# Kernel optimization log

Measured on AMD Instinct MI355X. Metric: run time of the kernel, lower is better.

## Reference

```python
import jax, jax.numpy as jnp
import numpy as np
import math

RANKS = [16, 8, 4, 2, 1]          # generate_mrlora_ranks(32 // 2)
LORA_ALPHA = 16.0
SCALES = [LORA_ALPHA / math.sqrt(r) for r in RANKS]  # use_rslora=True
D_IN = 4096
D_OUT = 4096


def setup_inputs() -> dict:
    key = jax.random.key(0)
    ks = jax.random.split(key, 3 + 2 * len(RANKS))
    x = jax.random.normal(ks[0], (4, 2048, D_IN), dtype=jnp.float32)
    W = jax.random.normal(ks[1], (D_OUT, D_IN), dtype=jnp.float32) * (1.0 / math.sqrt(D_IN))
    b = jax.random.normal(ks[2], (D_OUT,), dtype=jnp.float32) * 0.01
    inp = {"x": x, "W": W, "b": b}
    for i, r in enumerate(RANKS):
        # A: [r, D_IN], B: [D_OUT, r] (torch nn.Linear weight layout)
        inp[f"A{r}"] = jax.random.normal(ks[3 + 2 * i], (r, D_IN), dtype=jnp.float32) * (1.0 / math.sqrt(D_IN))
        inp[f"B{r}"] = jax.random.normal(ks[4 + 2 * i], (D_OUT, r), dtype=jnp.float32) * 0.02
    inp["alphas"] = jnp.ones((len(RANKS),), dtype=jnp.float32)
    return inp


def reference(x, W, b, A16, B16, A8, B8, A4, B4, A2, B2, A1, B1, alphas):
    # base linear: x @ W.T + b
    out = jnp.einsum('bsd,od->bso', x, W) + b
    As = [A16, A8, A4, A2, A1]
    Bs = [B16, B8, B4, B2, B1]
    # dropout p=0 -> identity; per-rank low-rank update with learned + rslora scale
    for i, (A, B) in enumerate(zip(As, Bs)):
        coef = alphas[i] * SCALES[i]
        out = out + coef * jnp.einsum('bsr,or->bso', jnp.einsum('bsd,rd->bsr', x, A), B)
    return out
```

## Files before the change

### kernel.cpp

```cpp
#include <hip/hip_runtime.h>
#include <hip/hip_bf16.h>
#include <stdint.h>

#define DK 4096
#define MROWS 8192
#define NOUT 4096
#define KP 4160
#define KP_B (KP*2)
#define NT 65

typedef __attribute__((ext_vector_type(8))) __bf16 bf16x8;
typedef __attribute__((ext_vector_type(4))) float f32x4;
typedef unsigned short u16;

struct __align__(8) us4 { u16 x, y, z, w; };

__device__ __forceinline__ u16 f2bf(float f) {
  union { float f; uint32_t u; } v; v.f = f;
  uint32_t r = v.u + 0x7fffu + ((v.u >> 16) & 1u);
  return (u16)(r >> 16);
}

__device__ __forceinline__ void gload16(const void* g, void* l) {
  __builtin_amdgcn_global_load_lds(
      (const __attribute__((address_space(1))) unsigned int*)g,
      (__attribute__((address_space(3))) unsigned int*)l, 16, 0, 0);
}

__global__ void conv_x(const float* __restrict__ x, u16* __restrict__ xb) {
  int m = blockIdx.x, t = threadIdx.x;
  const float* src = x + (size_t)m * DK;
  u16* dst = xb + (size_t)m * KP;
#pragma unroll
  for (int j = 0; j < 4; ++j) {
    int col = (t + j * 256) * 4;
    float4 v = *reinterpret_cast<const float4*>(src + col);
    us4 o = { f2bf(v.x), f2bf(v.y), f2bf(v.z), f2bf(v.w) };
    *reinterpret_cast<us4*>(dst + col) = o;
  }
  if (t < 64) dst[4096 + t] = 0;
}

__global__ void build_W(const float* __restrict__ W,
                        const float* __restrict__ B16, const float* __restrict__ B8,
                        const float* __restrict__ B4,  const float* __restrict__ B2,
                        const float* __restrict__ B1,  const float* __restrict__ alphas,
                        u16* __restrict__ wb) {
  int n = blockIdx.x, t = threadIdx.x;
  const float* src = W + (size_t)n * DK;
  u16* dst = wb + (size_t)n * KP;
#pragma unroll
  for (int j = 0; j < 4; ++j) {
    int col = (t + j * 256) * 4;
    float4 v = *reinterpret_cast<const float4*>(src + col);
    us4 o = { f2bf(v.x), f2bf(v.y), f2bf(v.z), f2bf(v.w) };
    *reinterpret_cast<us4*>(dst + col) = o;
  }
  if (t < 64) {
    u16 val = 0;
    if (t < 31) {
      float coef; const float* Bp; int r, rl;
      if (t < 16)      { coef = alphas[0] * 4.0f;                Bp = B16; r = 16; rl = t; }
      else if (t < 24) { coef = alphas[1] * 5.656854249492381f;  Bp = B8;  r = 8;  rl = t - 16; }
      else if (t < 28) { coef = alphas[2] * 8.0f;                Bp = B4;  r = 4;  rl = t - 24; }
      else if (t < 30) { coef = alphas[3] * 11.313708498984761f; Bp = B2;  r = 2;  rl = t - 28; }
      else             { coef = alphas[4] * 16.0f;               Bp = B1;  r = 1;  rl = 0; }
      val = f2bf(coef * Bp[(size_t)n * r + rl]);
    }
    dst[4096 + t] = val;
  }
}

__global__ void build_A(const float* __restrict__ A16, const float* __restrict__ A8,
                        const float* __restrict__ A4,  const float* __restrict__ A2,
                        const float* __restrict__ A1,  u16* __restrict__ ab) {
  int rr = blockIdx.x, t = threadIdx.x;
  const float* src = nullptr;
  if (rr < 16)      src = A16 + (size_t)rr * DK;
  else if (rr < 24) src = A8 + (size_t)(rr - 16) * DK;
  else if (rr < 28) src = A4 + (size_t)(rr - 24) * DK;
  else if (rr < 30) src = A2 + (size_t)(rr - 28) * DK;
  else if (rr < 31) src = A1;
  u16* dst = ab + (size_t)rr * DK;
#pragma unroll
  for (int j = 0; j < 4; ++j) {
    int col = (t + j * 256) * 4;
    us4 o = { 0, 0, 0, 0 };
    if (src) {
      float4 v = *reinterpret_cast<const float4*>(src + col);
      o = { f2bf(v.x), f2bf(v.y), f2bf(v.z), f2bf(v.w) };
    }
    *reinterpret_cast<us4*>(dst + col) = o;
  }
}

__global__ __launch_bounds__(256, 2) void xa_gemm(u16* xb, const u16* __restrict__ ab) {
  __shared__ u16 Xs[64 * 64];
  __shared__ u16 Qs[32 * 64];
  int m0 = blockIdx.x * 64;
  int t = threadIdx.x, lane = t & 63, w = t >> 6;
  int l15 = lane & 15, lg = lane >> 4;
  f32x4 acc[2] = {};
  const char* xbase = (const char*)xb + (size_t)m0 * KP_B;
  for (int kt = 0; kt < 64; ++kt) {
    size_t kb = (size_t)kt * 128;
    __syncthreads();
#pragma unroll
    for (int i = 0; i < 2; ++i) {
      int chunk = w * 2 + i;
      int off = chunk * 1024 + lane * 16;
      int row = off >> 7, colB = off & 127;
      gload16(xbase + (size_t)row * KP_B + kb + colB, (char*)Xs + chunk * 1024);
    }
    {
      int off = w * 1024 + lane * 16;
      int row = off >> 7, colB = off & 127;
      gload16((const char*)ab + (size_t)row * (DK * 2) + kb + colB, (char*)Qs + w * 1024);
    }
    asm volatile("s_waitcnt vmcnt(0)" ::: "memory");
    __syncthreads();
#pragma unroll
    for (int ks = 0; ks < 2; ++ks) {
      bf16x8 xf = *reinterpret_cast<const bf16x8*>((const char*)Xs + (w * 16 + l15) * 128 + ks * 64 + lg * 16);
#pragma unroll
      for (int ni = 0; ni < 2; ++ni) {
        bf16x8 af = *reinterpret_cast<const bf16x8*>((const char*)Qs + (ni * 16 + l15) * 128 + ks * 64 + lg * 16);
        acc[ni] = __builtin_amdgcn_mfma_f32_16x16x32_bf16(xf, af, acc[ni], 0, 0, 0);
      }
    }
  }
#pragma unroll
  for (int ni = 0; ni < 2; ++ni)
#pragma unroll
    for (int r = 0; r < 4; ++r) {
      int m = m0 + w * 16 + lg * 4 + r;
      int c = 4096 + ni * 16 + l15;
      xb[(size_t)m * KP + c] = f2bf(acc[ni][r]);
    }
}

__device__ __forceinline__ void stage_tile(const char* gbase, char* lbase, int w, int lane, int i) {
  int chunk = (w << 2) + i;
  int row = (chunk << 3) + (lane >> 3);
  int src_c = ((lane & 7) ^ (lane >> 3)) << 4;
  gload16(gbase + (size_t)row * KP_B + src_c, lbase + chunk * 1024);
}

__device__ __forceinline__ bf16x8 rdfrag(const char* base, int row, int cb) {
  return *reinterpret_cast<const bf16x8*>(base + row * 128 + (cb ^ ((row & 7) << 4)));
}

__global__ __launch_bounds__(512, 2) void gemm_main(const u16* __restrict__ xb, const u16* __restrict__ wb,
                                                    const float* __restrict__ bias, float* __restrict__ out) {
  __shared__ u16 As0[256 * 64], As1[256 * 64];
  __shared__ u16 Bs0[256 * 64], Bs1[256 * 64];
  int bid = blockIdx.x;
  int swz = (bid & 7) * 64 + (bid >> 3);
  int mt = swz >> 4, nt = swz & 15;
  int m0 = mt * 256, n0 = nt * 256;
  int t = threadIdx.x, lane = t & 63, w = t >> 6;
  int wr = w >> 2, wc = w & 3;
  int l15 = lane & 15, lg = lane >> 4;

  f32x4 acc[8][4] = {};
  bf16x8 af[4][2], bl[2][2], bh[2][2];

  const char* Ag = (const char*)xb + (size_t)m0 * KP_B;
  const char* Bg = (const char*)wb + (size_t)n0 * KP_B;
  char *AcA = (char*)As0, *AnA = (char*)As1, *AcB = (char*)Bs0, *AnB = (char*)Bs1;

#pragma unroll
  for (int i = 0; i < 4; ++i) stage_tile(Bg, AcB, w, lane, i);
#pragma unroll
  for (int i = 0; i < 4; ++i) stage_tile(Ag, AcA, w, lane, i);
#pragma unroll
  for (int i = 0; i < 4; ++i) stage_tile(Bg + 128, AnB, w, lane, i);
  asm volatile("s_waitcnt vmcnt(4)" ::: "memory");
  __builtin_amdgcn_s_barrier();

  const int Arow = wr * 128 + l15;
  const int Brow = wc * 64 + l15;
  const int cb0 = lg * 16;

  for (int kt = 0; kt < NT; ++kt) {
    const char* Agk1 = Ag + (size_t)(kt + 1) * 128;
    const char* Bgk2 = Bg + (size_t)(kt + 2) * 128;
    const bool doA = (kt + 1 < NT), doB = (kt + 2 < NT);

#pragma unroll
    for (int mi = 0; mi < 4; ++mi)
#pragma unroll
      for (int ks = 0; ks < 2; ++ks)
        af[mi][ks] = rdfrag(AcA, Arow + mi * 16, cb0 + ks * 64);
#pragma unroll
    for (int ni = 0; ni < 2; ++ni)
#pragma unroll
      for (int ks = 0; ks < 2; ++ks)
        bl[ni][ks] = rdfrag(AcB, Brow + ni * 16, cb0 + ks * 64);
#pragma unroll
    for (int ni = 0; ni < 2; ++ni)
#pragma unroll
      for (int ks = 0; ks < 2; ++ks)
        bh[ni][ks] = rdfrag(AcB, Brow + 32 + ni * 16, cb0 + ks * 64);
    if (doA) {
      stage_tile(Agk1, AnA, w, lane, 0); stage_tile(Agk1, AnA, w, lane, 1);
      stage_tile(Agk1, AnA, w, lane, 2); stage_tile(Agk1, AnA, w, lane, 3);
    }
    asm volatile("s_waitcnt lgkmcnt(8)" ::: "memory");
    __builtin_amdgcn_s_barrier();
    asm volatile("s_waitcnt lgkmcnt(0)" ::: "memory");
    __builtin_amdgcn_sched_barrier(0);
    __builtin_amdgcn_s_setprio(1);
#pragma unroll
    for (int mi = 0; mi < 4; ++mi)
#pragma unroll
      for (int ni = 0; ni < 2; ++ni)
#pragma unroll
        for (int ks = 0; ks < 2; ++ks)
          acc[mi][ni] = __builtin_amdgcn_mfma_f32_16x16x32_bf16(af[mi][ks], bl[ni][ks], acc[mi][ni], 0, 0, 0);
#pragma unroll
    for (int mi = 0; mi < 4; ++mi)
#pragma unroll
      for (int ni = 0; ni < 2; ++ni)
#pragma unroll
        for (int ks = 0; ks < 2; ++ks)
          acc[mi][ni + 2] = __builtin_amdgcn_mfma_f32_16x16x32_bf16(af[mi][ks], bh[ni][ks], acc[mi][ni + 2], 0, 0, 0);
    __builtin_amdgcn_s_setprio(0);
    __builtin_amdgcn_s_barrier();

#pragma unroll
    for (int mi = 0; mi < 4; ++mi)
#pragma unroll
      for (int ks = 0; ks < 2; ++ks)
        af[mi][ks] = rdfrag(AcA, Arow + 64 + mi * 16, cb0 + ks * 64);
    if (doB) {
      stage_tile(Bgk2, AcB, w, lane, 0); stage_tile(Bgk2, AcB, w, lane, 1);
      stage_tile(Bgk2, AcB, w, lane, 2); stage_tile(Bgk2, AcB, w, lane, 3);
    }
    __builtin_amdgcn_s_barrier();
    asm volatile("s_waitcnt lgkmcnt(0)" ::: "memory");
    __builtin_amdgcn_sched_barrier(0);
    __builtin_amdgcn_s_setprio(1);
#pragma unroll
    for (int mi = 0; mi < 4; ++mi)
#pragma unroll
      for (int ni = 0; ni < 2; ++ni)
#pragma unroll
        for (int ks = 0; ks < 2; ++ks)
          acc[mi + 4][ni + 2] = __builtin_amdgcn_mfma_f32_16x16x32_bf16(af[mi][ks], bh[ni][ks], acc[mi + 4][ni + 2], 0, 0, 0);
#pragma unroll
    for (int mi = 0; mi < 4; ++mi)
#pragma unroll
      for (int ni = 0; ni < 2; ++ni)
#pragma unroll
        for (int ks = 0; ks < 2; ++ks)
          acc[mi + 4][ni] = __builtin_amdgcn_mfma_f32_16x16x32_bf16(af[mi][ks], bl[ni][ks], acc[mi + 4][ni], 0, 0, 0);
    __builtin_amdgcn_s_setprio(0);
    if (kt < NT - 2) asm volatile("s_waitcnt vmcnt(4)" ::: "memory");
    else             asm volatile("s_waitcnt vmcnt(0)" ::: "memory");
    __builtin_amdgcn_s_barrier();

    { char* tp = AcA; AcA = AnA; AnA = tp; }
    { char* tp = AcB; AcB = AnB; AnB = tp; }
  }

  float bn[4];
#pragma unroll
  for (int ni = 0; ni < 4; ++ni) bn[ni] = bias[n0 + wc * 64 + ni * 16 + l15];
#pragma unroll
  for (int mi = 0; mi < 8; ++mi) {
    int mbase = m0 + wr * 128 + mi * 16 + lg * 4;
#pragma unroll
    for (int ni = 0; ni < 4; ++ni) {
      int n = n0 + wc * 64 + ni * 16 + l15;
#pragma unroll
      for (int r = 0; r < 4; ++r)
        out[(size_t)(mbase + r) * NOUT + n] = acc[mi][ni][r] + bn[ni];
    }
  }
}

extern "C" void kernel_launch(void* const* d_in, const int* in_sizes, int n_in,
                              void* d_out, int out_size, void* d_ws, size_t ws_size,
                              hipStream_t stream) {
  const float* x   = (const float*)d_in[0];
  const float* W   = (const float*)d_in[1];
  const float* b   = (const float*)d_in[2];
  const float* A16 = (const float*)d_in[3];
  const float* B16 = (const float*)d_in[4];
  const float* A8  = (const float*)d_in[5];
  const float* B8  = (const float*)d_in[6];
  const float* A4  = (const float*)d_in[7];
  const float* B4  = (const float*)d_in[8];
  const float* A2  = (const float*)d_in[9];
  const float* B2  = (const float*)d_in[10];
  const float* A1  = (const float*)d_in[11];
  const float* B1  = (const float*)d_in[12];
  const float* alphas = (const float*)d_in[13];

  char* ws = (char*)d_ws;
  u16* xb = (u16*)ws;
  u16* wb = (u16*)(ws + 68157440);
  u16* ab = (u16*)(ws + 68157440 + 34078720);
  float* out = (float*)d_out;

  conv_x<<<MROWS, 256, 0, stream>>>(x, xb);
  build_W<<<NOUT, 256, 0, stream>>>(W, B16, B8, B4, B2, B1, alphas, wb);
  build_A<<<32, 256, 0, stream>>>(A16, A8, A4, A2, A1, ab);
  xa_gemm<<<MROWS / 64, 256, 0, stream>>>(xb, ab);
  gemm_main<<<(MROWS / 256) * (NOUT / 256), 512, 0, stream>>>(xb, wb, b, out);
}
```

Measured before the change: 325.8 us.

## Restructure GEMM main loop to single-barrier double buffering with interleaved LDS reads

Replaces the staggered A(k+1)/B(k+2) prefetch scheme, which used several barriers per K-step, with a simple double buffer. Both A and B for the next K-tile are staged into the alternate buffers, and there is one barrier per iteration. The second half of the A fragments is read into a separate register set (af2) while the first MFMA groups run, so LDS reads overlap compute instead of sitting behind barriers. The cost is more VGPRs and a full vmcnt(0) wait each iteration, so the global prefetch is only one tile ahead, which may expose memory latency.

```diff
diff --git a/kernel.cpp b/kernel.cpp
--- a/kernel.cpp
+++ b/kernel.cpp
@@ -163,19 +163,17 @@
   int l15 = lane & 15, lg = lane >> 4;
 
   f32x4 acc[8][4] = {};
-  bf16x8 af[4][2], bl[2][2], bh[2][2];
+  bf16x8 af[4][2], af2[4][2], bl[2][2], bh[2][2];
 
   const char* Ag = (const char*)xb + (size_t)m0 * KP_B;
   const char* Bg = (const char*)wb + (size_t)n0 * KP_B;
   char *AcA = (char*)As0, *AnA = (char*)As1, *AcB = (char*)Bs0, *AnB = (char*)Bs1;
 
 #pragma unroll
+  for (int i = 0; i < 4; ++i) stage_tile(Ag, AcA, w, lane, i);
+#pragma unroll
   for (int i = 0; i < 4; ++i) stage_tile(Bg, AcB, w, lane, i);
-#pragma unroll
-  for (int i = 0; i < 4; ++i) stage_tile(Ag, AcA, w, lane, i);
-#pragma unroll
-  for (int i = 0; i < 4; ++i) stage_tile(Bg + 128, AnB, w, lane, i);
-  asm volatile("s_waitcnt vmcnt(4)" ::: "memory");
+  asm volatile("s_waitcnt vmcnt(0)" ::: "memory");
   __builtin_amdgcn_s_barrier();
 
   const int Arow = wr * 128 + l15;
@@ -184,8 +182,8 @@
 
   for (int kt = 0; kt < NT; ++kt) {
     const char* Agk1 = Ag + (size_t)(kt + 1) * 128;
-    const char* Bgk2 = Bg + (size_t)(kt + 2) * 128;
-    const bool doA = (kt + 1 < NT), doB = (kt + 2 < NT);
+    const char* Bgk1 = Bg + (size_t)(kt + 1) * 128;
+    const bool doS = (kt + 1 < NT);
 
 #pragma unroll
     for (int mi = 0; mi < 4; ++mi)
@@ -197,17 +195,49 @@
 #pragma unroll
       for (int ks = 0; ks < 2; ++ks)
         bl[ni][ks] = rdfrag(AcB, Brow + ni * 16, cb0 + ks * 64);
+    if (doS) {
+      stage_tile(Agk1, AnA, w, lane, 0); stage_tile(Agk1, AnA, w, lane, 1);
+      stage_tile(Agk1, AnA, w, lane, 2); stage_tile(Agk1, AnA, w, lane, 3);
+    }
+
 #pragma unroll
     for (int ni = 0; ni < 2; ++ni)
 #pragma unroll
       for (int ks = 0; ks < 2; ++ks)
         bh[ni][ks] = rdfrag(AcB, Brow + 32 + ni * 16, cb0 + ks * 64);
-    if (doA) {
-      stage_tile(Agk1, AnA, w, lane, 0); stage_tile(Agk1, AnA, w, lane, 1);
-      stage_tile(Agk1, AnA, w, lane, 2); stage_tile(Agk1, AnA, w, lane, 3);
-    }
+    if (doS) {
+      stage_tile(Bgk1, AnB, w, lane, 0); stage_tile(Bgk1, AnB, w, lane, 1);
+      stage_tile(Bgk1, AnB, w, lane, 2); stage_tile(Bgk1, AnB, w, lane, 3);
+    }
+    asm volatile("s_waitcnt lgkmcnt(4)" ::: "memory");
+    __builtin_amdgcn_sched_barrier(0);
+    __builtin_amdgcn_s_setprio(1);
+#pragma unroll
+    for (int mi = 0; mi < 4; ++mi)
+#pragma unroll
+      for (int ni = 0; ni < 2; ++ni)
+#pragma unroll
+        for (int ks = 0; ks < 2; ++ks)
+          acc[mi][ni] = __builtin_amdgcn_mfma_f32_16x16x32_bf16(af[mi][ks], bl[ni][ks], acc[mi][ni], 0, 0, 0);
+    __builtin_amdgcn_s_setprio(0);
+
+#pragma unroll
+    for (int mi = 0; mi < 4; ++mi)
+#pragma unroll
+      for (int ks = 0; ks < 2; ++ks)
+        af2[mi][ks] = rdfrag(AcA, Arow + 64 + mi * 16, cb0 + ks * 64);
     asm volatile("s_waitcnt lgkmcnt(8)" ::: "memory");
-    __builtin_amdgcn_s_barrier();
+    __builtin_amdgcn_sched_barrier(0);
+    __builtin_amdgcn_s_setprio(1);
+#pragma unroll
+    for (int mi = 0; mi < 4; ++mi)
+#pragma unroll
+      for (int ni = 0; ni < 2; ++ni)
+#pragma unroll
+        for (int ks = 0; ks < 2; ++ks)
+          acc[mi][ni + 2] = __builtin_amdgcn_mfma_f32_16x16x32_bf16(af[mi][ks], bh[ni][ks], acc[mi][ni + 2], 0, 0, 0);
+    __builtin_amdgcn_s_setprio(0);
+
     asm volatile("s_waitcnt lgkmcnt(0)" ::: "memory");
     __builtin_amdgcn_sched_barrier(0);
     __builtin_amdgcn_s_setprio(1);
@@ -217,47 +247,19 @@
       for (int ni = 0; ni < 2; ++ni)
 #pragma unroll
         for (int ks = 0; ks < 2; ++ks)
-          acc[mi][ni] = __builtin_amdgcn_mfma_f32_16x16x32_bf16(af[mi][ks], bl[ni][ks], acc[mi][ni], 0, 0, 0);
+          acc[mi + 4][ni + 2] = __builtin_amdgcn_mfma_f32_16x16x32_bf16(af2[mi][ks], bh[ni][ks], acc[mi + 4][ni + 2], 0, 0, 0);
+    __builtin_amdgcn_s_setprio(0);
+
+    __builtin_amdgcn_s_setprio(1);
 #pragma unroll
     for (int mi = 0; mi < 4; ++mi)
 #pragma unroll
       for (int ni = 0; ni < 2; ++ni)
 #pragma unroll
         for (int ks = 0; ks < 2; ++ks)
-          acc[mi][ni + 2] = __builtin_amdgcn_mfma_f32_16x16x32_bf16(af[mi][ks], bh[ni][ks], acc[mi][ni + 2], 0, 0, 0);
+          acc[mi + 4][ni] = __builtin_amdgcn_mfma_f32_16x16x32_bf16(af2[mi][ks], bl[ni][ks], acc[mi + 4][ni], 0, 0, 0);
     __builtin_amdgcn_s_setprio(0);
-    __builtin_amdgcn_s_barrier();
-
-#pragma unroll
-    for (int mi = 0; mi < 4; ++mi)
-#pragma unroll
-      for (int ks = 0; ks < 2; ++ks)
-        af[mi][ks] = rdfrag(AcA, Arow + 64 + mi * 16, cb0 + ks * 64);
-    if (doB) {
-      stage_tile(Bgk2, AcB, w, lane, 0); stage_tile(Bgk2, AcB, w, lane, 1);
-      stage_tile(Bgk2, AcB, w, lane, 2); stage_tile(Bgk2, AcB, w, lane, 3);
-    }
-    __builtin_amdgcn_s_barrier();
-    asm volatile("s_waitcnt lgkmcnt(0)" ::: "memory");
-    __builtin_amdgcn_sched_barrier(0);
-    __builtin_amdgcn_s_setprio(1);
-#pragma unroll
-    for (int mi = 0; mi < 4; ++mi)
-#pragma unroll
-      for (int ni = 0; ni < 2; ++ni)
-#pragma unroll
-        for (int ks = 0; ks < 2; ++ks)
-          acc[mi + 4][ni + 2] = __builtin_amdgcn_mfma_f32_16x16x32_bf16(af[mi][ks], bh[ni][ks], acc[mi + 4][ni + 2], 0, 0, 0);
-#pragma unroll
-    for (int mi = 0; mi < 4; ++mi)
-#pragma unroll
-      for (int ni = 0; ni < 2; ++ni)
-#pragma unroll
-        for (int ks = 0; ks < 2; ++ks)
-          acc[mi + 4][ni] = __builtin_amdgcn_mfma_f32_16x16x32_bf16(af[mi][ks], bl[ni][ks], acc[mi + 4][ni], 0, 0, 0);
-    __builtin_amdgcn_s_setprio(0);
-    if (kt < NT - 2) asm volatile("s_waitcnt vmcnt(4)" ::: "memory");
-    else             asm volatile("s_waitcnt vmcnt(0)" ::: "memory");
+    asm volatile("s_waitcnt vmcnt(0)" ::: "memory");
     __builtin_amdgcn_s_barrier();
 
     { char* tp = AcA; AcA = AnA; AnA = tp; }
```

After: 316.3 us. 1.03x faster.
